# Optimization experiments

Hardware: AMD Instinct MI355X
Metric: run time of the kernel (lower is better)

Reference implementation:

```python
import jax, jax.numpy as jnp
import numpy as np

INFTY_APPROX = 1e+30
ROTARY_BASE = 10000.0
D_HEAD = 128


def rope(x):
    # x: [B, H, T, D]
    *_, length, width = x.shape
    half = width // 2
    positions = jnp.arange(length)[:, None].astype(x.dtype)          # [T, 1]
    dims = jnp.arange(half).astype(x.dtype)                           # [half]
    ang_freqs = jnp.power(ROTARY_BASE, -dims / half)[None, :]         # [1, half]
    radians = positions * ang_freqs                                   # [T, half]
    cos = jnp.cos(radians)[None, None].astype(x.dtype)                # [1,1,T,half]
    sin = jnp.sin(radians)[None, None].astype(x.dtype)
    even, odd = jnp.split(x, 2, axis=-1)
    r_even = even * cos - odd * sin
    r_odd = even * sin + odd * cos
    return jnp.concatenate([r_even, r_odd], axis=-1)


def setup_inputs() -> dict:
    key = jax.random.key(0)
    ks = jax.random.split(key, 5)
    B, T, M, D = 4, 2048, 1024, D_HEAD
    H = M // D
    x = jax.random.normal(ks[0], (B, T, M), dtype=jnp.float32)
    scale = M ** -0.5
    wq = jax.random.normal(ks[1], (H, M, D), dtype=jnp.float32) * scale
    wk = jax.random.normal(ks[2], (H, M, D), dtype=jnp.float32) * scale
    wv = jax.random.normal(ks[3], (H, M, D), dtype=jnp.float32) * scale
    wo = jax.random.normal(ks[4], (H, D, M), dtype=jnp.float32) * scale
    return {"x": x, "wq": wq, "wk": wk, "wv": wv, "wo": wo}


def reference(x, wq, wk, wv, wo):
    # x: [B, T, M]; w{q,k,v}: [H, M, D]; wo: [H, D, M]
    q = jnp.einsum('bim,hmd->bhid', x, wq)
    k = jnp.einsum('bim,hmd->bhid', x, wk)
    v = jnp.einsum('bim,hmd->bhid', x, wv)
    q = rope(q)
    k = rope(k)
    # NOTE: module scales BOTH q and k by d_head**-0.5 (mup-style 1/d overall)
    mult = jnp.asarray(D_HEAD ** -0.5, dtype=x.dtype)
    s = jnp.einsum('bhid,bhjd->bhij', q * mult, k * mult)
    T = s.shape[-1]
    i = jnp.arange(T)[:, None]
    j = jnp.arange(T)[None, :]
    mask = (i < j).astype(s.dtype)[None, None]  # future positions masked
    s = s - jnp.asarray(INFTY_APPROX, dtype=s.dtype) * mask
    p = jax.nn.softmax(s, axis=-1)
    o = jnp.einsum('bhij,bhjd->bhid', p, v)
    r = jnp.einsum('bhid,hdm->bim', o, wo)
    return r
```

## Files before the change

### kernel.cpp

```cpp
#include <hip/hip_runtime.h>
#include <math.h>


typedef unsigned short u16;
typedef __attribute__((ext_vector_type(8))) short short8;
typedef __attribute__((ext_vector_type(4))) float floatx4;

#define MFMA_B16(a, b, c) __builtin_amdgcn_mfma_f32_16x16x32_bf16((a), (b), (c), 0, 0, 0)

__device__ __forceinline__ void async_cp16(const void* g, void* l) {
  __builtin_amdgcn_global_load_lds(
      (const __attribute__((address_space(1))) unsigned int*)g,
      (__attribute__((address_space(3))) unsigned int*)l, 16, 0, 0);
}

__device__ __forceinline__ u16 f2bf(float f) {
  unsigned u = __float_as_uint(f);
  u += 0x7FFFu + ((u >> 16) & 1u);
  return (u16)(u >> 16);
}

__device__ __forceinline__ int swz8(int row, int chunk) { return ((chunk ^ (row & 7)) << 3); }


__global__ void conv_x(const float* __restrict__ xf, u16* __restrict__ xb) {
  int idx = (blockIdx.x * 256 + threadIdx.x) * 4;
  float4 v = *(const float4*)(xf + idx);
  ushort4 o = make_ushort4(f2bf(v.x), f2bf(v.y), f2bf(v.z), f2bf(v.w));
  *(ushort4*)(xb + idx) = o;
}

__global__ void prep_wqkv(const float* __restrict__ wq, const float* __restrict__ wk,
                          const float* __restrict__ wv, u16* __restrict__ wT) {
  __shared__ float tile[32][33];
  const float* src = (blockIdx.z == 0) ? wq : (blockIdx.z == 1) ? wk : wv;
  u16* dst = wT + (size_t)blockIdx.z * 1024 * 1024;
  int h = blockIdx.y >> 2, dt = blockIdx.y & 3;
  int m0 = blockIdx.x * 32, d0 = dt * 32;
  int tx = threadIdx.x, ty = threadIdx.y;
#pragma unroll
  for (int i = 0; i < 4; i++) {
    int r = ty + i * 8;
    tile[r][tx] = src[((size_t)h * 1024 + m0 + r) * 128 + d0 + tx];
  }
  __syncthreads();
#pragma unroll
  for (int i = 0; i < 4; i++) {
    int r = ty + i * 8;
    dst[((size_t)h * 128 + d0 + r) * 1024 + m0 + tx] = f2bf(tile[tx][r]);
  }
}

__global__ void prep_wo(const float* __restrict__ wo, u16* __restrict__ woT) {
  __shared__ float tile[32][33];
  int r0 = blockIdx.y * 32, c0 = blockIdx.x * 32;
  int tx = threadIdx.x, ty = threadIdx.y;
#pragma unroll
  for (int i = 0; i < 4; i++) {
    int r = ty + i * 8;
    tile[r][tx] = wo[(size_t)(r0 + r) * 1024 + c0 + tx];
  }
  __syncthreads();
#pragma unroll
  for (int i = 0; i < 4; i++) {
    int r = ty + i * 8;
    woT[(size_t)(c0 + r) * 1024 + r0 + tx] = f2bf(tile[tx][r]);
  }
}

__global__ void prep_rope(float2* __restrict__ tab) {
  int idx = blockIdx.x * 256 + threadIdx.x;
  int t = idx >> 6, d = idx & 63;
  const float c1 = -0.20762050593046015f;
  float freq = exp2f((float)d * c1);
  float rad = (float)t * freq;
  float s, c;
  sincosf(rad, &s, &c);
  tab[idx] = make_float2(c, s);
}

template <int MODE>
__launch_bounds__(256, 2)
__global__ void gemm_bt(const u16* __restrict__ A, const u16* __restrict__ Bt,
                        void* __restrict__ out0, u16* __restrict__ out_k,
                        u16* __restrict__ out_v, const float2* __restrict__ ropetab) {
  __shared__ u16 smem[16384];
  u16* As = smem;
  u16* Bs = smem + 8192;
  const int tid = threadIdx.x;
  const int w = tid >> 6, lane = tid & 63, quad = lane >> 4, l15 = lane & 15;
  const int row0 = blockIdx.x * 128;
  const int by = blockIdx.y;
  const int n0 = by * 128;

  floatx4 acc[2][8] = {};

  for (int kt = 0; kt < 16; ++kt) {
    __syncthreads();
#pragma unroll
    for (int i = 0; i < 4; i++) {
      int cidx = (w * 4 + i) * 64 + lane;
      int r = cidx >> 3, c = cidx & 7, cg = c ^ (r & 7);
      async_cp16(A + (size_t)(row0 + r) * 1024 + kt * 64 + cg * 8, As + (w * 4 + i) * 512);
      async_cp16(Bt + (size_t)(n0 + r) * 1024 + kt * 64 + cg * 8, Bs + (w * 4 + i) * 512);
    }
    __syncthreads();
#pragma unroll
    for (int ks = 0; ks < 2; ks++) {
      short8 af[2];
#pragma unroll
      for (int mi = 0; mi < 2; mi++) {
        int r = w * 32 + mi * 16 + l15;
        af[mi] = *(const short8*)(As + r * 64 + swz8(r, ks * 4 + quad));
      }
#pragma unroll
      for (int ni = 0; ni < 8; ni++) {
        int n = ni * 16 + l15;
        short8 bf = *(const short8*)(Bs + n * 64 + swz8(n, ks * 4 + quad));
        acc[0][ni] = MFMA_B16(af[0], bf, acc[0][ni]);
        acc[1][ni] = MFMA_B16(af[1], bf, acc[1][ni]);
      }
    }
  }
  __syncthreads();

  if (MODE == 0) {
    int sel = by >> 3, h = by & 7;
    if (sel < 2) {
      u16* dst = sel ? out_k : (u16*)out0;
#pragma unroll
      for (int mi = 0; mi < 2; mi++) {
#pragma unroll
        for (int reg = 0; reg < 4; reg++) {
          int row = row0 + w * 32 + mi * 16 + quad * 4 + reg;
          int b = row >> 11, t = row & 2047;
          u16* drow = dst + ((size_t)(b * 8 + h) * 2048 + t) * 128;
#pragma unroll
          for (int ni = 0; ni < 4; ni++) {
            int d = ni * 16 + l15;
            float2 cs = ropetab[t * 64 + d];
            float e = acc[mi][ni][reg], o = acc[mi][ni + 4][reg];
            drow[d] = f2bf(e * cs.x - o * cs.y);
            drow[d + 64] = f2bf(e * cs.y + o * cs.x);
          }
        }
      }
    } else {
#pragma unroll
      for (int mi = 0; mi < 2; mi++) {
#pragma unroll
        for (int reg = 0; reg < 4; reg++) {
          int r = w * 32 + mi * 16 + quad * 4 + reg;
#pragma unroll
          for (int ni = 0; ni < 8; ni++) {
            int col = ni * 16 + l15;
            smem[r * 128 + swz8(r, col >> 3) + (col & 7)] = f2bf(acc[mi][ni][reg]);
          }
        }
      }
      __syncthreads();
      int tl = tid & 127, dg = tid >> 7;
      int row = row0 + tl;
      int b = row >> 11, t = row & 2047;
      u16* vdst = out_v + (size_t)(b * 8 + h) * 128 * 2048;
#pragma unroll
      for (int dd = 0; dd < 64; dd++) {
        int d = dg * 64 + dd;
        u16 val = smem[tl * 128 + swz8(tl, d >> 3) + (d & 7)];
        vdst[(size_t)d * 2048 + t] = val;
      }
    }
  } else {
    float* outf = (float*)out0;
#pragma unroll
    for (int mi = 0; mi < 2; mi++) {
#pragma unroll
      for (int reg = 0; reg < 4; reg++) {
        int row = row0 + w * 32 + mi * 16 + quad * 4 + reg;
#pragma unroll
        for (int ni = 0; ni < 8; ni++) {
          outf[(size_t)row * 1024 + n0 + ni * 16 + l15] = acc[mi][ni][reg];
        }
      }
    }
  }
}

__device__ __forceinline__ void stage_kv(const u16* kb, const u16* vb, int jt,
                                         u16* Kd, u16* Vd, int w, int lane) {
#pragma unroll
  for (int i = 0; i < 4; i++) {
    int cidx = (w * 4 + i) * 64 + lane;
    int rK = cidx >> 4, cK = cidx & 15, gK = cK ^ (rK & 7);
    async_cp16(kb + (size_t)(jt * 64 + rK) * 128 + gK * 8, Kd + (w * 4 + i) * 512);
    int rV = cidx >> 3, cV = cidx & 7, gV = cV ^ (rV & 7);
    async_cp16(vb + (size_t)rV * 2048 + jt * 64 + gV * 8, Vd + (w * 4 + i) * 512);
  }
}

__launch_bounds__(256, 4)
__global__ void flash_attn(const u16* __restrict__ Q, const u16* __restrict__ Kw,
                           const u16* __restrict__ Vw, u16* __restrict__ O) {
  __shared__ u16 Ks[64 * 128];
  __shared__ u16 Vs[128 * 64];
  __shared__ u16 Ps[64 * 64];
  const int tid = threadIdx.x;
  const int w = tid >> 6, lane = tid & 63, quad = lane >> 4, l15 = lane & 15;
  const int bh = blockIdx.y;
  const int qt = (int)((blockIdx.x + bh) & 31);
  const int i0 = qt * 64;
  const u16* qb = Q + (size_t)bh * 2048 * 128;
  const u16* kb = Kw + (size_t)bh * 2048 * 128;
  const u16* vb = Vw + (size_t)bh * 128 * 2048;
  const int b = bh >> 3, h = bh & 7;
  const float SC = 0.011271055f;

  short8 qf[4];
  {
    int qrow = i0 + w * 16 + l15;
#pragma unroll
    for (int ks = 0; ks < 4; ks++)
      qf[ks] = *(const short8*)(qb + (size_t)qrow * 128 + ks * 32 + quad * 8);
  }

  floatx4 accO[8] = {};
  float lrow[4] = {0.f, 0.f, 0.f, 0.f};

  stage_kv(kb, vb, 0, Ks, Vs, w, lane);

  for (int jt = 0; jt <= qt; ++jt) {
    __syncthreads();
    const bool diag = (jt == qt);

    floatx4 sa[4] = {};
#pragma unroll
    for (int jj = 0; jj < 4; jj++) {
      if (diag && jj > w) continue;
#pragma unroll
      for (int ks = 0; ks < 4; ks++) {
        int j = jj * 16 + l15;
        short8 bfr = *(const short8*)(Ks + j * 128 + swz8(j, ks * 4 + quad));
        sa[jj] = MFMA_B16(qf[ks], bfr, sa[jj]);
      }
    }

#pragma unroll
    for (int jj = 0; jj < 4; jj++) {
#pragma unroll
      for (int r = 0; r < 4; r++) {
        float s = sa[jj][r] * SC;
        if (diag) {
          int jg = jj * 16 + l15;
          int ig = w * 16 + quad * 4 + r;
          if (jg > ig) s = -1e30f;
        }
        float p = exp2f(s);
        lrow[r] += p;
        int pr = w * 16 + quad * 4 + r;
        int col = jj * 16 + l15;
        Ps[pr * 64 + swz8(pr, col >> 3) + (col & 7)] = f2bf(p);
      }
    }

#pragma unroll
    for (int k2 = 0; k2 < 2; k2++) {
      int prow = w * 16 + l15;
      short8 pa = *(const short8*)(Ps + prow * 64 + swz8(prow, k2 * 4 + quad));
#pragma unroll
      for (int nt = 0; nt < 8; nt++) {
        int dr = nt * 16 + l15;
        short8 vf = *(const short8*)(Vs + dr * 64 + swz8(dr, k2 * 4 + quad));
        accO[nt] = MFMA_B16(pa, vf, accO[nt]);
      }
    }

    __syncthreads();
    if (jt < qt) stage_kv(kb, vb, jt + 1, Ks, Vs, w, lane);
  }

#pragma unroll
  for (int off = 1; off < 16; off <<= 1)
#pragma unroll
    for (int r = 0; r < 4; r++) lrow[r] += __shfl_xor(lrow[r], off);

#pragma unroll
  for (int nt = 0; nt < 8; nt++) {
#pragma unroll
    for (int r = 0; r < 4; r++) {
      int t = i0 + w * 16 + quad * 4 + r;
      float ov = accO[nt][r] / fmaxf(lrow[r], 1e-30f);
      O[(((size_t)b * 2048 + t) * 8 + h) * 128 + nt * 16 + l15] = f2bf(ov);
    }
  }
}

extern "C" void kernel_launch(void* const* d_in, const int* in_sizes, int n_in,
                              void* d_out, int out_size, void* d_ws, size_t ws_size,
                              hipStream_t stream) {
  const float* x = (const float*)d_in[0];
  const float* wq = (const float*)d_in[1];
  const float* wk = (const float*)d_in[2];
  const float* wv = (const float*)d_in[3];
  const float* wo = (const float*)d_in[4];
  float* out = (float*)d_out;

  char* ws = (char*)d_ws;
  const size_t SZ = 16777216;
  u16* x_bf = (u16*)(ws);
  u16* q_ws = (u16*)(ws + SZ);
  u16* k_ws = (u16*)(ws + 2 * SZ);
  u16* v_ws = (u16*)(ws + 3 * SZ);
  u16* o_ws = (u16*)(ws + 4 * SZ);
  u16* wT = (u16*)(ws + 5 * SZ);
  u16* woT = (u16*)(ws + 5 * SZ + 6291456);
  float2* tab = (float2*)(ws + 5 * SZ + 6291456 + 2097152);

  conv_x<<<8192, 256, 0, stream>>>(x, x_bf);
  prep_wqkv<<<dim3(32, 32, 3), dim3(32, 8), 0, stream>>>(wq, wk, wv, wT);
  prep_wo<<<dim3(32, 32), dim3(32, 8), 0, stream>>>(wo, woT);
  prep_rope<<<512, 256, 0, stream>>>(tab);
  gemm_bt<0><<<dim3(64, 24), 256, 0, stream>>>(x_bf, wT, q_ws, k_ws, v_ws, tab);
  flash_attn<<<dim3(32, 32), 256, 0, stream>>>(q_ws, k_ws, v_ws, o_ws);
  gemm_bt<1><<<dim3(64, 8), 256, 0, stream>>>(o_ws, woT, out, nullptr, nullptr, nullptr);
}
```

Before: 264.6 us.

## Restructure flash attention to 128-row query tiles with double-buffered KV staging

The attention kernel now gives each block 128 query rows (32 per wave as two MFMA row tiles), so every staged K/V tile feeds twice as much compute. K/V staging is double-buffered, with the next tile prefetched before the current one is computed. It also computes S transposed so P can be packed with v_cvt_pk_bf16, raises MFMA priority with s_setprio, and orders the 1D grid to pair short and long causal tiles for load balance. In exchange the block uses more LDS and registers, occupancy drops to 2 blocks per SIMD, and there are half as many blocks.

Measured after the change: 256.5 us. -3.1%, faster.

```diff
diff --git a/kernel.cpp b/kernel.cpp
--- a/kernel.cpp
+++ b/kernel.cpp
@@ -18,6 +18,12 @@
   unsigned u = __float_as_uint(f);
   u += 0x7FFFu + ((u >> 16) & 1u);
   return (u16)(u >> 16);
+}
+
+__device__ __forceinline__ unsigned cvt_pk_bf16(float lo, float hi) {
+  unsigned r;
+  asm("v_cvt_pk_bf16_f32 %0, %1, %2" : "=v"(r) : "v"(lo), "v"(hi));
+  return r;
 }
 
 __device__ __forceinline__ int swz8(int row, int chunk) { return ((chunk ^ (row & 7)) << 3); }
@@ -198,98 +204,139 @@
   }
 }
 
-__launch_bounds__(256, 4)
+__launch_bounds__(256, 2)
 __global__ void flash_attn(const u16* __restrict__ Q, const u16* __restrict__ Kw,
                            const u16* __restrict__ Vw, u16* __restrict__ O) {
-  __shared__ u16 Ks[64 * 128];
-  __shared__ u16 Vs[128 * 64];
-  __shared__ u16 Ps[64 * 64];
+  __shared__ u16 smem[40960];
+  u16* const Ps = smem + 32768;
+
   const int tid = threadIdx.x;
   const int w = tid >> 6, lane = tid & 63, quad = lane >> 4, l15 = lane & 15;
-  const int bh = blockIdx.y;
-  const int qt = (int)((blockIdx.x + bh) & 31);
-  const int i0 = qt * 64;
+
+  const int id = (int)blockIdx.x;
+  const int bh = id & 31;
+  const int p = (id >> 5) & 7;
+  const int qt = (id >> 8) ? (15 - p) : p;
+
   const u16* qb = Q + (size_t)bh * 2048 * 128;
   const u16* kb = Kw + (size_t)bh * 2048 * 128;
   const u16* vb = Vw + (size_t)bh * 128 * 2048;
   const int b = bh >> 3, h = bh & 7;
   const float SC = 0.011271055f;
 
-  short8 qf[4];
-  {
-    int qrow = i0 + w * 16 + l15;
+  const int iw = qt * 128 + w * 32;
+  const int nj = 2 * qt + 2;
+
+  short8 qf[2][4];
+#pragma unroll
+  for (int mi = 0; mi < 2; mi++) {
+    int qrow = iw + mi * 16 + l15;
 #pragma unroll
     for (int ks = 0; ks < 4; ks++)
-      qf[ks] = *(const short8*)(qb + (size_t)qrow * 128 + ks * 32 + quad * 8);
-  }
-
-  floatx4 accO[8] = {};
-  float lrow[4] = {0.f, 0.f, 0.f, 0.f};
-
-  stage_kv(kb, vb, 0, Ks, Vs, w, lane);
-
-  for (int jt = 0; jt <= qt; ++jt) {
+      qf[mi][ks] = *(const short8*)(qb + (size_t)qrow * 128 + ks * 32 + quad * 8);
+  }
+
+  floatx4 accO[2][8] = {};
+  float lsum[2] = {0.f, 0.f};
+
+  stage_kv(kb, vb, 0, smem, smem + 16384, w, lane);
+
+  int cur = 0;
+  for (int jt = 0; jt < nj; ++jt) {
     __syncthreads();
-    const bool diag = (jt == qt);
-
-    floatx4 sa[4] = {};
-#pragma unroll
-    for (int jj = 0; jj < 4; jj++) {
-      if (diag && jj > w) continue;
-#pragma unroll
-      for (int ks = 0; ks < 4; ks++) {
-        int j = jj * 16 + l15;
-        short8 bfr = *(const short8*)(Ks + j * 128 + swz8(j, ks * 4 + quad));
-        sa[jj] = MFMA_B16(qf[ks], bfr, sa[jj]);
-      }
-    }
-
-#pragma unroll
-    for (int jj = 0; jj < 4; jj++) {
-#pragma unroll
-      for (int r = 0; r < 4; r++) {
-        float s = sa[jj][r] * SC;
-        if (diag) {
-          int jg = jj * 16 + l15;
-          int ig = w * 16 + quad * 4 + r;
-          if (jg > ig) s = -1e30f;
-        }
-        float p = exp2f(s);
-        lrow[r] += p;
-        int pr = w * 16 + quad * 4 + r;
-        int col = jj * 16 + l15;
-        Ps[pr * 64 + swz8(pr, col >> 3) + (col & 7)] = f2bf(p);
-      }
-    }
-
-#pragma unroll
-    for (int k2 = 0; k2 < 2; k2++) {
-      int prow = w * 16 + l15;
-      short8 pa = *(const short8*)(Ps + prow * 64 + swz8(prow, k2 * 4 + quad));
+
+    if (jt + 1 < nj)
+      stage_kv(kb, vb, jt + 1, smem + (cur ^ 1) * 8192, smem + 16384 + (cur ^ 1) * 8192, w, lane);
+
+    const u16* Ks = smem + cur * 8192;
+    const u16* Vs = smem + 16384 + cur * 8192;
+    const int j0 = jt * 64;
+
+    if (j0 <= iw + 31) {
+      const bool partial = (j0 + 63 > iw);
+
+      floatx4 sa[4][2] = {};
+      __builtin_amdgcn_s_setprio(1);
+#pragma unroll
+      for (int jj = 0; jj < 4; jj++) {
+        const bool ok1 = (j0 + jj * 16 <= iw + 31);
+        if (!ok1) continue;
+        const bool ok0 = (j0 + jj * 16 <= iw + 15);
+#pragma unroll
+        for (int ks = 0; ks < 4; ks++) {
+          int j = jj * 16 + l15;
+          short8 kf = *(const short8*)(Ks + j * 128 + swz8(j, ks * 4 + quad));
+          if (ok0) sa[jj][0] = MFMA_B16(kf, qf[0][ks], sa[jj][0]);
+          sa[jj][1] = MFMA_B16(kf, qf[1][ks], sa[jj][1]);
+        }
+      }
+      __builtin_amdgcn_s_setprio(0);
+
+#pragma unroll
+      for (int mi = 0; mi < 2; mi++) {
+        const int prow = w * 32 + mi * 16 + l15;
+        const int ig = iw + mi * 16 + l15;
+#pragma unroll
+        for (int jj = 0; jj < 4; jj++) {
+          float pv[4];
+#pragma unroll
+          for (int r = 0; r < 4; r++) {
+            float s = sa[jj][mi][r] * SC;
+            if (partial) {
+              int jg = j0 + jj * 16 + quad * 4 + r;
+              if (jg > ig) s = -1e30f;
+            }
+            pv[r] = exp2f(s);
+            lsum[mi] += pv[r];
+          }
+          uint2 pk;
+          pk.x = cvt_pk_bf16(pv[0], pv[1]);
+          pk.y = cvt_pk_bf16(pv[2], pv[3]);
+          int jc = jj * 16 + quad * 4;
+          *(uint2*)(Ps + prow * 64 + swz8(prow, jc >> 3) + (jc & 7)) = pk;
+        }
+      }
+
+      __builtin_amdgcn_s_setprio(1);
+#pragma unroll
+      for (int k2 = 0; k2 < 2; k2++) {
+        short8 pa[2];
+#pragma unroll
+        for (int mi = 0; mi < 2; mi++) {
+          int prow = w * 32 + mi * 16 + l15;
+          pa[mi] = *(const short8*)(Ps + prow * 64 + swz8(prow, k2 * 4 + quad));
+        }
+#pragma unroll
+        for (int nt = 0; nt < 8; nt++) {
+          int dr = nt * 16 + l15;
+          short8 vf = *(const short8*)(Vs + dr * 64 + swz8(dr, k2 * 4 + quad));
+          accO[0][nt] = MFMA_B16(pa[0], vf, accO[0][nt]);
+          accO[1][nt] = MFMA_B16(pa[1], vf, accO[1][nt]);
+        }
+      }
+      __builtin_amdgcn_s_setprio(0);
+    }
+    cur ^= 1;
+  }
+
+#pragma unroll
+  for (int mi = 0; mi < 2; mi++) {
+    lsum[mi] += __shfl_xor(lsum[mi], 16);
+    lsum[mi] += __shfl_xor(lsum[mi], 32);
+  }
+
+#pragma unroll
+  for (int mi = 0; mi < 2; mi++) {
+#pragma unroll
+    for (int r = 0; r < 4; r++) {
+      float lr = __shfl(lsum[mi], quad * 4 + r);
+      float inv = 1.0f / fmaxf(lr, 1e-30f);
+      int t = iw + mi * 16 + quad * 4 + r;
 #pragma unroll
       for (int nt = 0; nt < 8; nt++) {
-        int dr = nt * 16 + l15;
-        short8 vf = *(const short8*)(Vs + dr * 64 + swz8(dr, k2 * 4 + quad));
-        accO[nt] = MFMA_B16(pa, vf, accO[nt]);
-      }
-    }
-
-    __syncthreads();
-    if (jt < qt) stage_kv(kb, vb, jt + 1, Ks, Vs, w, lane);
-  }
-
-#pragma unroll
-  for (int off = 1; off < 16; off <<= 1)
-#pragma unroll
-    for (int r = 0; r < 4; r++) lrow[r] += __shfl_xor(lrow[r], off);
-
-#pragma unroll
-  for (int nt = 0; nt < 8; nt++) {
-#pragma unroll
-    for (int r = 0; r < 4; r++) {
-      int t = i0 + w * 16 + quad * 4 + r;
-      float ov = accO[nt][r] / fmaxf(lrow[r], 1e-30f);
-      O[(((size_t)b * 2048 + t) * 8 + h) * 128 + nt * 16 + l15] = f2bf(ov);
+        O[(((size_t)b * 2048 + t) * 8 + h) * 128 + nt * 16 + l15] =
+            f2bf(accO[mi][nt][r] * inv);
+      }
     }
   }
 }
@@ -320,6 +367,6 @@
   prep_wo<<<dim3(32, 32), dim3(32, 8), 0, stream>>>(wo, woT);
   prep_rope<<<512, 256, 0, stream>>>(tab);
   gemm_bt<0><<<dim3(64, 24), 256, 0, stream>>>(x_bf, wT, q_ws, k_ws, v_ws, tab);
-  flash_attn<<<dim3(32, 32), 256, 0, stream>>>(q_ws, k_ws, v_ws, o_ws);
+  flash_attn<<<512, 256, 0, stream>>>(q_ws, k_ws, v_ws, o_ws);
   gemm_bt<1><<<dim3(64, 8), 256, 0, stream>>>(o_ws, woT, out, nullptr, nullptr, nullptr);
 }
```
